# Performance work log

Measured on AMD Instinct MI355X. Metric: run time of the kernel, lower is better.

Reference implementation:

```python
import jax, jax.numpy as jnp
import numpy as np
from jax import lax

B, CIN, COUT, H, W, K = 8, 256, 256, 64, 64, 3
KK = K * K
PAD, STRIDE = 1, 1
EPS = 1e-5


def setup_inputs() -> dict:
    key = jax.random.key(0)
    k0, k1, k2 = jax.random.split(key, 3)
    x = jax.random.normal(k0, (B, CIN, H, W), jnp.float32)
    # offset/mask predicting conv: 3*K*K output channels (o1, o2, mask)
    w_off = jax.random.normal(k1, (3 * KK, CIN, K, K), jnp.float32) * 0.01
    b_off = jnp.zeros((3 * KK,), jnp.float32)
    # main deformable conv weight
    weight = jax.random.normal(k2, (COUT, CIN, K, K), jnp.float32) / np.sqrt(CIN * KK).astype(np.float32)
    bias = jnp.zeros((COUT,), jnp.float32)
    gamma = jnp.ones((COUT,), jnp.float32)
    beta = jnp.zeros((COUT,), jnp.float32)
    return {"x": x, "w_off": w_off, "b_off": b_off, "weight": weight,
            "bias": bias, "gamma": gamma, "beta": beta}


def _bilinear_sample(img, ph, pw):
    """img: [C,H,W]; ph,pw: [KK,H,W] float sample positions. Zero outside. -> [C,KK,H,W]"""
    h0 = jnp.floor(ph).astype(jnp.int32)
    w0 = jnp.floor(pw).astype(jnp.int32)
    h1, w1 = h0 + 1, w0 + 1
    lh = ph - h0.astype(ph.dtype)
    lw = pw - w0.astype(pw.dtype)
    hh, hw = 1.0 - lh, 1.0 - lw

    def corner(hi, wi):
        valid = (hi >= 0) & (hi < H) & (wi >= 0) & (wi < W)
        hc = jnp.clip(hi, 0, H - 1)
        wc = jnp.clip(wi, 0, W - 1)
        v = img[:, hc, wc]  # [C,KK,H,W]
        return v * valid.astype(img.dtype)[None]

    return (corner(h0, w0) * (hh * hw)[None] + corner(h0, w1) * (hh * lw)[None]
            + corner(h1, w0) * (lh * hw)[None] + corner(h1, w1) * (lh * lw)[None])


def _forward(x, w_off, b_off, weight, bias, gamma, beta):
    dn = ('NCHW', 'OIHW', 'NCHW')
    # offset/mask branch (standard conv)
    om = lax.conv_general_dilated(x, w_off, (STRIDE, STRIDE), ((PAD, PAD), (PAD, PAD)),
                                  dimension_numbers=dn) + b_off[None, :, None, None]
    o1, o2, m = jnp.split(om, 3, axis=1)
    offset = jnp.concatenate([o1, o2], axis=1)          # [B, 2*KK, H, W]
    off_h = offset[:, 0::2]                             # [B, KK, H, W] dy per tap
    off_w = offset[:, 1::2]                             # [B, KK, H, W] dx per tap
    mask = jax.nn.sigmoid(m)                            # [B, KK, H, W]

    taps = jnp.arange(KK)
    base_h = (taps // K - PAD).astype(jnp.float32)[:, None, None] \
        + (jnp.arange(H, dtype=jnp.float32) * STRIDE)[None, :, None]  # [KK,H,1]
    base_w = (taps % K - PAD).astype(jnp.float32)[:, None, None] \
        + (jnp.arange(W, dtype=jnp.float32) * STRIDE)[None, None, :]  # [KK,1,W]
    ph = base_h[None] + off_h                           # [B,KK,H,W]
    pw = base_w[None] + off_w

    sampled = jax.vmap(_bilinear_sample)(x, ph, pw)     # [B,CIN,KK,H,W]
    sampled = sampled * mask[:, None]                   # modulated (DCNv2)

    y = jnp.einsum('bckhw,ock->bohw', sampled, weight.reshape(COUT, CIN, KK))
    y = y + bias[None, :, None, None]

    # BatchNorm2d (training mode: batch statistics) + ReLU
    mean = y.mean(axis=(0, 2, 3))
    var = y.var(axis=(0, 2, 3))
    yn = (y - mean[None, :, None, None]) * lax.rsqrt(var + EPS)[None, :, None, None]
    out = jax.nn.relu(gamma[None, :, None, None] * yn + beta[None, :, None, None])
    return out


def reference(x, w_off, b_off, weight, bias, gamma, beta):
    return _forward(x, w_off, b_off, weight, bias, gamma, beta)
```

## Files before the change

### kernel.cpp

```cpp
#include <hip/hip_runtime.h>
#include <cstdint>

#define BB    8
#define CIN   256
#define COUT  256
#define HH    64
#define WW    64
#define HWSZ  4096
#define NPIX  32768
#define NTAP  9

typedef __attribute__((ext_vector_type(8))) short    s16x8;
typedef __attribute__((ext_vector_type(8))) unsigned short u16x8;
typedef __attribute__((ext_vector_type(4))) unsigned short u16x4;
typedef __attribute__((ext_vector_type(4))) float    f32x4;

__device__ __forceinline__ float bf2f(unsigned short u) {
    unsigned int v = ((unsigned int)u) << 16;
    return __builtin_bit_cast(float, v);
}
__device__ __forceinline__ unsigned short f2bf(float f) {
    unsigned int u = __builtin_bit_cast(unsigned int, f);
    unsigned int r = (u + 0x7FFFu + ((u >> 16) & 1u)) >> 16;
    return (unsigned short)r;
}

__global__ void k_pack_x(const float* __restrict__ x, unsigned short* __restrict__ xT) {
    int blk = blockIdx.x;
    int b    = blk & 7;
    int rest = blk >> 3;
    int h    = rest >> 2;
    int c0   = (rest & 3) * 64;
    __shared__ float tile[64][65];
    int t = threadIdx.x;
#pragma unroll
    for (int r = 0; r < 16; ++r) {
        int idx = t + r * 256;
        int i = idx >> 6, w = idx & 63;
        tile[i][w] = x[(((b * 256 + c0 + i) * 64 + h) * 64) + w];
    }
    __syncthreads();
#pragma unroll
    for (int r = 0; r < 2; ++r) {
        int idx = t + r * 256;
        int w  = idx >> 3;
        int c8 = (idx & 7) * 8;
        u16x8 res;
#pragma unroll
        for (int k = 0; k < 8; ++k) res[k] = f2bf(tile[c8 + k][w]);
        *reinterpret_cast<u16x8*>(&xT[((b * 64 + h) * 64 + w) * 256 + c0 + c8]) = res;
    }
}

__global__ void k_pack_w2(const float* __restrict__ w, const float* __restrict__ woff,
                          unsigned short* __restrict__ wT, unsigned short* __restrict__ wofT) {
    int bid = blockIdx.x;
    int t = threadIdx.x;
    if (bid < 2304) {
        int idx = bid * 256 + t;
        int j   = idx & 7;
        int q   = (idx >> 3) & 3;
        int o16 = (idx >> 5) & 15;
        int n16 = (idx >> 9) & 15;
        int kc  = (idx >> 13) & 7;
        int tp  = idx >> 16;
        int c = kc * 32 + q * 8 + j;
        int o = n16 * 16 + o16;
        wT[idx] = f2bf(w[(o * 256 + c) * 9 + tp]);
    } else {
        int idx = (bid - 2304) * 256 + t;
        int c  = idx & 255;
        int j  = (idx >> 8) & 31;
        int tp = idx >> 13;
        float v = (j < 27) ? woff[(j * 256 + c) * 9 + tp] : 0.f;
        wofT[idx] = f2bf(v);
    }
}

__global__ __launch_bounds__(256, 2)
void k_offconv(const unsigned short* __restrict__ xT,
               const unsigned short* __restrict__ wofT,
               const float* __restrict__ b_off,
               float* __restrict__ om) {
    int blk = blockIdx.x;
    int b = blk & 7, h = blk >> 3;
    int P0 = (b * 64 + h) * 64;
    int t = threadIdx.x;
    int lane = t & 63, wv = t >> 6;
    int p0w = wv * 16;
    int lm = lane & 15, q = lane >> 4;
    __shared__ unsigned short S3[3 * 66 * 136];

    const f32x4 FZ = {0.f, 0.f, 0.f, 0.f};
    f32x4 acc0 = FZ, acc1 = FZ;

    for (int cc = 0; cc < 2; ++cc) {
        __syncthreads();
        if (t < 96) {
            int rr = t >> 5, col = (t >> 4) & 1, c8 = (t & 15) * 8;
            u16x8 z = {0,0,0,0,0,0,0,0};
            *reinterpret_cast<u16x8*>(&S3[(rr * 66 + col * 65) * 136 + c8]) = z;
        }
#pragma unroll
        for (int r = 0; r < 12; ++r) {
            int v = t + r * 256;
            int rr = v >> 10, rem = v & 1023;
            int w = rem >> 4, c8 = (rem & 15) * 8;
            int hr = h + rr - 1;
            u16x8 d = {0,0,0,0,0,0,0,0};
            if (hr >= 0 && hr < 64)
                d = *reinterpret_cast<const u16x8*>(xT + ((b * 64 + hr) * 64 + w) * 256 + cc * 128 + c8);
            *reinterpret_cast<u16x8*>(&S3[(rr * 66 + w + 1) * 136 + c8]) = d;
        }
        __syncthreads();
#pragma unroll
        for (int tp = 0; tp < 9; ++tp) {
            int dh = tp / 3, dw = tp % 3;
            const unsigned short* wb = wofT + (tp * 32 + lm) * 256 + cc * 128;
#pragma unroll
            for (int kc = 0; kc < 4; ++kc) {
                s16x8 a = *reinterpret_cast<const s16x8*>(&S3[(dh * 66 + p0w + lm + dw) * 136 + kc * 32 + q * 8]);
                s16x8 b0 = *reinterpret_cast<const s16x8*>(wb + kc * 32 + q * 8);
                s16x8 b1 = *reinterpret_cast<const s16x8*>(wb + 16 * 256 + kc * 32 + q * 8);
                acc0 = __builtin_amdgcn_mfma_f32_16x16x32_bf16(a, b0, acc0, 0, 0, 0);
                acc1 = __builtin_amdgcn_mfma_f32_16x16x32_bf16(a, b1, acc1, 0, 0, 0);
            }
        }
    }
#pragma unroll
    for (int n = 0; n < 2; ++n) {
        int j = n * 16 + lm;
        float bj = (j < 27) ? b_off[j] : 0.f;
        f32x4 a = n ? acc1 : acc0;
#pragma unroll
        for (int i = 0; i < 4; ++i) {
            int prow = p0w + q * 4 + i;
            om[(P0 + prow) * 32 + j] = a[i] + bj;
        }
    }
}

__global__ __launch_bounds__(512, 4)
void k_main(const unsigned short* __restrict__ xT,
            const unsigned short* __restrict__ wTk,
            const float* __restrict__ om,
            const float* __restrict__ bias,
            unsigned short* __restrict__ y16,
            float* __restrict__ gsum, float* __restrict__ gssq) {
    int blk = blockIdx.x;
    int b = blk & 7, h = blk >> 3;
    int pblk = b * 64 + h;
    int P0 = pblk * 64;
    int t = threadIdx.x;
    int lane = t & 63, wv = t >> 6;
    int lm = lane & 15, q = lane >> 4;

    __shared__ unsigned short S[2][64 * 264];
    __shared__ float OMS[64 * 33];

    {
        int v = t * 4;
        int p = v >> 5, j = v & 31;
        float4 tmp = *reinterpret_cast<const float4*>(om + P0 * 32 + v);
        OMS[p * 33 + j]     = tmp.x;
        OMS[p * 33 + j + 1] = tmp.y;
        OMS[p * 33 + j + 2] = tmp.z;
        OMS[p * 33 + j + 3] = tmp.w;
    }
    __syncthreads();

    if (wv >= 4) {
        int pw = wv - 4;
        int s  = lane & 7;
        int pA = pw * 16 + (lane >> 3);
        int pB = pA + 8;
        int rb = b * 4096;

        float wgA[4], wgB[4];
        int   adA[4], adB[4];

        auto setup = [&](int tp, int p, float* wg, int* ad) {
            float oh = OMS[p * 33 + 2 * tp];
            float ow = OMS[p * 33 + 2 * tp + 1];
            float mv = OMS[p * 33 + 18 + tp];
            float mk = 1.f / (1.f + __expf(-mv));
            float ph = (float)(h + tp / 3 - 1) + oh;
            float pw_ = (float)(p + tp % 3 - 1) + ow;
            float fh0 = floorf(ph), fw0 = floorf(pw_);
            int ih0 = (int)fh0, iw0 = (int)fw0;
            float lh = ph - fh0, lw = pw_ - fw0;
            float hh = 1.f - lh, hw_ = 1.f - lw;
            bool vh0 = (ih0 >= 0) & (ih0 < 64);
            bool vh1 = (ih0 + 1 >= 0) & (ih0 + 1 < 64);
            bool vw0 = (iw0 >= 0) & (iw0 < 64);
            bool vw1 = (iw0 + 1 >= 0) & (iw0 + 1 < 64);
            wg[0] = hh * hw_ * mk * (float)(vh0 & vw0);
            wg[1] = hh * lw  * mk * (float)(vh0 & vw1);
            wg[2] = lh * hw_ * mk * (float)(vh1 & vw0);
            wg[3] = lh * lw  * mk * (float)(vh1 & vw1);
            int ch0 = min(max(ih0, 0), 63), ch1 = min(max(ih0 + 1, 0), 63);
            int cw0 = min(max(iw0, 0), 63), cw1 = min(max(iw0 + 1, 0), 63);
            ad[0] = ((rb + ch0 * 64 + cw0) * 256);
            ad[1] = ((rb + ch0 * 64 + cw1) * 256);
            ad[2] = ((rb + ch1 * 64 + cw0) * 256);
            ad[3] = ((rb + ch1 * 64 + cw1) * 256);
        };

        u16x8 rP[4], rQ[4];
        auto issueSet = [&](const int* ad, int j, u16x8* r) {
            int off = j * 64 + s * 8;
#pragma unroll
            for (int c = 0; c < 4; ++c)
                r[c] = *reinterpret_cast<const u16x8*>(xT + ad[c] + off);
        };
        auto blendSet = [&](int buf, int p, const float* wg, int j, u16x8* r) {
            u16x8 res;
#pragma unroll
            for (int k = 0; k < 8; ++k) {
                float v = wg[0] * bf2f(r[0][k]);
                v = fmaf(wg[1], bf2f(r[1][k]), v);
                v = fmaf(wg[2], bf2f(r[2][k]), v);
                v = fmaf(wg[3], bf2f(r[3][k]), v);
                res[k] = f2bf(v);
            }
            *reinterpret_cast<u16x8*>(&S[buf][p * 264 + j * 64 + s * 8]) = res;
        };
        auto fillTap = [&](int tp, int buf) {
            setup(tp, pA, wgA, adA);
            setup(tp, pB, wgB, adB);
            issueSet(adA, 0, rP);
            issueSet(adA, 1, rQ);
            blendSet(buf, pA, wgA, 0, rP);  issueSet(adA, 2, rP);
            blendSet(buf, pA, wgA, 1, rQ);  issueSet(adA, 3, rQ);
            blendSet(buf, pA, wgA, 2, rP);  issueSet(adB, 0, rP);
            blendSet(buf, pA, wgA, 3, rQ);  issueSet(adB, 1, rQ);
            blendSet(buf, pB, wgB, 0, rP);  issueSet(adB, 2, rP);
            blendSet(buf, pB, wgB, 1, rQ);  issueSet(adB, 3, rQ);
            blendSet(buf, pB, wgB, 2, rP);
            blendSet(buf, pB, wgB, 3, rQ);
        };

        fillTap(0, 0);
        __syncthreads();
        for (int tp = 0; tp < 9; ++tp) {
            if (tp < 8) fillTap(tp + 1, (tp + 1) & 1);
            __syncthreads();
        }
    } else {
        int o0 = wv * 64;
        const f32x4 FZ = {0.f, 0.f, 0.f, 0.f};
        f32x4 acc[4][4];
#pragma unroll
        for (int m = 0; m < 4; ++m)
#pragma unroll
            for (int n = 0; n < 4; ++n) acc[m][n] = FZ;

        __syncthreads();
        for (int tp = 0; tp < 9; ++tp) {
            const unsigned short* Sc = &S[tp & 1][0];
            const unsigned short* wtap = wTk + (size_t)tp * 65536
                                       + (size_t)(wv * 4) * 512 + lm * 32 + q * 8;
            s16x8 wbuf[2][4];
#pragma unroll
            for (int n = 0; n < 4; ++n)
                wbuf[0][n] = *reinterpret_cast<const s16x8*>(wtap + n * 512);
#pragma unroll
            for (int kc = 0; kc < 8; ++kc) {
                if (kc < 7) {
                    const unsigned short* wb = wtap + (kc + 1) * 8192;
#pragma unroll
                    for (int n = 0; n < 4; ++n)
                        wbuf[(kc + 1) & 1][n] = *reinterpret_cast<const s16x8*>(wb + n * 512);
                }
#pragma unroll
                for (int mt = 0; mt < 4; ++mt) {
                    s16x8 a = *reinterpret_cast<const s16x8*>(
                        &Sc[(mt * 16 + lm) * 264 + kc * 32 + q * 8]);
#pragma unroll
                    for (int n = 0; n < 4; ++n)
                        acc[mt][n] = __builtin_amdgcn_mfma_f32_16x16x32_bf16(
                            a, wbuf[kc & 1][n], acc[mt][n], 0, 0, 0);
                }
            }
            __syncthreads();
        }

        u16x4* yv = reinterpret_cast<u16x4*>(y16);
#pragma unroll
        for (int nt = 0; nt < 4; ++nt) {
            int o = o0 + nt * 16 + lm;
            float bo = bias[o];
            float sacc = 0.f, ssacc = 0.f;
#pragma unroll
            for (int mt = 0; mt < 4; ++mt) {
                u16x4 st;
#pragma unroll
                for (int i = 0; i < 4; ++i) {
                    float v = acc[mt][nt][i] + bo;
                    st[i] = f2bf(v);
                    sacc += v; ssacc += v * v;
                }
                int idx4 = ((pblk * 4 + wv) * 16 + nt * 4 + mt) * 64 + lane;
                yv[idx4] = st;
            }
            sacc  += __shfl_xor(sacc, 16);
            sacc  += __shfl_xor(sacc, 32);
            ssacc += __shfl_xor(ssacc, 16);
            ssacc += __shfl_xor(ssacc, 32);
            if (q == 0) {
                atomicAdd(&gsum[o], sacc);
                atomicAdd(&gssq[o], ssacc);
            }
        }
    }
}

__global__ void k_bnrelu(const unsigned short* __restrict__ y16,
                         const float* __restrict__ gsum, const float* __restrict__ gssq,
                         const float* __restrict__ gamma, const float* __restrict__ beta,
                         float* __restrict__ out) {
    int blk = blockIdx.x;
    int b = blk & 7, h = blk >> 3;
    int pblk = b * 64 + h;
    __shared__ unsigned short T[64 * 257];
    __shared__ float sc[256], sh[256];
    int t = threadIdx.x;
    {
        const float n = 32768.f;
        float mean = gsum[t] / n;
        float var = gssq[t] / n - mean * mean;
        float inv = rsqrtf(var + 1e-5f);
        float s = gamma[t] * inv;
        sc[t] = s;
        sh[t] = beta[t] - mean * s;
    }
    const u16x4* yv = reinterpret_cast<const u16x4*>(y16) + pblk * 4096;
#pragma unroll
    for (int r = 0; r < 16; ++r) {
        int v = t + r * 256;
        u16x4 d = yv[v];
        int lane = v & 63, mt = (v >> 6) & 3, nt = (v >> 8) & 3, wvv = (v >> 10) & 3;
        int p = mt * 16 + (lane >> 4) * 4;
        int o = wvv * 64 + nt * 16 + (lane & 15);
        T[(p + 0) * 257 + o] = d[0];
        T[(p + 1) * 257 + o] = d[1];
        T[(p + 2) * 257 + o] = d[2];
        T[(p + 3) * 257 + o] = d[3];
    }
    __syncthreads();
    int w4   = (t & 15) * 4;
    int orow = t >> 4;
    float* obase = out + (size_t)b * (256 * 4096) + h * 64;
#pragma unroll
    for (int it = 0; it < 16; ++it) {
        int o = orow + it * 16;
        float scl = sc[o], shf = sh[o];
        float4 vo;
        vo.x = fmaxf(bf2f(T[(w4 + 0) * 257 + o]) * scl + shf, 0.f);
        vo.y = fmaxf(bf2f(T[(w4 + 1) * 257 + o]) * scl + shf, 0.f);
        vo.z = fmaxf(bf2f(T[(w4 + 2) * 257 + o]) * scl + shf, 0.f);
        vo.w = fmaxf(bf2f(T[(w4 + 3) * 257 + o]) * scl + shf, 0.f);
        *reinterpret_cast<float4*>(obase + (size_t)o * 4096 + w4) = vo;
    }
}

extern "C" void kernel_launch(void* const* d_in, const int* in_sizes, int n_in,
                              void* d_out, int out_size, void* d_ws, size_t ws_size,
                              hipStream_t stream) {
    const float* x      = (const float*)d_in[0];
    const float* w_off  = (const float*)d_in[1];
    const float* b_off  = (const float*)d_in[2];
    const float* weight = (const float*)d_in[3];
    const float* bias   = (const float*)d_in[4];
    const float* gamma  = (const float*)d_in[5];
    const float* beta   = (const float*)d_in[6];

    char* ws = (char*)d_ws;
    const size_t OFF_XT    = 0;
    const size_t OFF_WT    = OFF_XT + 16777216;
    const size_t OFF_WOFT  = OFF_WT + 1179648;
    const size_t OFF_OM    = OFF_WOFT + 147456;
    const size_t OFF_Y16   = OFF_OM + 4194304;
    const size_t OFF_SUM   = OFF_Y16 + 16777216;
    const size_t OFF_SUMSQ = OFF_SUM + 1024;

    unsigned short* xT   = (unsigned short*)(ws + OFF_XT);
    unsigned short* wTk  = (unsigned short*)(ws + OFF_WT);
    unsigned short* wofT = (unsigned short*)(ws + OFF_WOFT);
    float* om    = (float*)(ws + OFF_OM);
    unsigned short* y16  = (unsigned short*)(ws + OFF_Y16);
    float* sum   = (float*)(ws + OFF_SUM);
    float* sumsq = (float*)(ws + OFF_SUMSQ);

    hipMemsetAsync(ws + OFF_SUM, 0, 2048, stream);

    k_pack_x <<<2048, 256, 0, stream>>>(x, xT);
    k_pack_w2<<<2592, 256, 0, stream>>>(weight, w_off, wTk, wofT);
    k_offconv<<< 512, 256, 0, stream>>>(xT, wofT, b_off, om);
    k_main   <<< 512, 512, 0, stream>>>(xT, wTk, om, bias, y16, sum, sumsq);
    k_bnrelu <<< 512, 256, 0, stream>>>(y16, sum, sumsq, gamma, beta, (float*)d_out);
}
```

Measured before the change: 211.4 us.

## Fuse offset conv into main kernel and merge pack kernels

```diff
diff --git a/kernel.cpp b/kernel.cpp
--- a/kernel.cpp
+++ b/kernel.cpp
@@ -6,9 +6,6 @@
 #define COUT  256
 #define HH    64
 #define WW    64
-#define HWSZ  4096
-#define NPIX  32768
-#define NTAP  9
 
 typedef __attribute__((ext_vector_type(8))) short    s16x8;
 typedef __attribute__((ext_vector_type(8))) unsigned short u16x8;
@@ -25,39 +22,39 @@
     return (unsigned short)r;
 }
 
-__global__ void k_pack_x(const float* __restrict__ x, unsigned short* __restrict__ xT) {
+__global__ void k_pack(const float* __restrict__ x,
+                       const float* __restrict__ w,
+                       const float* __restrict__ woff,
+                       unsigned short* __restrict__ xT,
+                       unsigned short* __restrict__ wTk,
+                       unsigned short* __restrict__ wofT) {
     int blk = blockIdx.x;
-    int b    = blk & 7;
-    int rest = blk >> 3;
-    int h    = rest >> 2;
-    int c0   = (rest & 3) * 64;
-    __shared__ float tile[64][65];
     int t = threadIdx.x;
-#pragma unroll
-    for (int r = 0; r < 16; ++r) {
-        int idx = t + r * 256;
-        int i = idx >> 6, w = idx & 63;
-        tile[i][w] = x[(((b * 256 + c0 + i) * 64 + h) * 64) + w];
-    }
-    __syncthreads();
-#pragma unroll
-    for (int r = 0; r < 2; ++r) {
-        int idx = t + r * 256;
-        int w  = idx >> 3;
-        int c8 = (idx & 7) * 8;
-        u16x8 res;
-#pragma unroll
-        for (int k = 0; k < 8; ++k) res[k] = f2bf(tile[c8 + k][w]);
-        *reinterpret_cast<u16x8*>(&xT[((b * 64 + h) * 64 + w) * 256 + c0 + c8]) = res;
-    }
-}
-
-__global__ void k_pack_w2(const float* __restrict__ w, const float* __restrict__ woff,
-                          unsigned short* __restrict__ wT, unsigned short* __restrict__ wofT) {
-    int bid = blockIdx.x;
-    int t = threadIdx.x;
-    if (bid < 2304) {
-        int idx = bid * 256 + t;
+    __shared__ float tile[64 * 65];
+    if (blk < 2048) {
+        int b    = blk & 7;
+        int rest = blk >> 3;
+        int h    = rest >> 2;
+        int c0   = (rest & 3) * 64;
+#pragma unroll
+        for (int r = 0; r < 16; ++r) {
+            int idx = t + r * 256;
+            int i = idx >> 6, w_ = idx & 63;
+            tile[i * 65 + w_] = x[(((b * 256 + c0 + i) * 64 + h) * 64) + w_];
+        }
+        __syncthreads();
+#pragma unroll
+        for (int r = 0; r < 2; ++r) {
+            int idx = t + r * 256;
+            int w_ = idx >> 3;
+            int c8 = (idx & 7) * 8;
+            u16x8 res;
+#pragma unroll
+            for (int k = 0; k < 8; ++k) res[k] = f2bf(tile[(c8 + k) * 65 + w_]);
+            *reinterpret_cast<u16x8*>(&xT[((b * 64 + h) * 64 + w_) * 256 + c0 + c8]) = res;
+        }
+    } else if (blk < 4352) {
+        int idx = (blk - 2048) * 256 + t;
         int j   = idx & 7;
         int q   = (idx >> 3) & 3;
         int o16 = (idx >> 5) & 15;
@@ -66,108 +63,95 @@
         int tp  = idx >> 16;
         int c = kc * 32 + q * 8 + j;
         int o = n16 * 16 + o16;
-        wT[idx] = f2bf(w[(o * 256 + c) * 9 + tp]);
+        wTk[idx] = f2bf(w[(o * 256 + c) * 9 + tp]);
     } else {
-        int idx = (bid - 2304) * 256 + t;
+        int idx = (blk - 4352) * 256 + t;
         int c  = idx & 255;
         int j  = (idx >> 8) & 31;
         int tp = idx >> 13;
-        float v = (j < 27) ? woff[(j * 256 + c) * 9 + tp] : 0.f;
-        wofT[idx] = f2bf(v);
-    }
-}
-
-__global__ __launch_bounds__(256, 2)
-void k_offconv(const unsigned short* __restrict__ xT,
-               const unsigned short* __restrict__ wofT,
-               const float* __restrict__ b_off,
-               float* __restrict__ om) {
-    int blk = blockIdx.x;
-    int b = blk & 7, h = blk >> 3;
-    int P0 = (b * 64 + h) * 64;
-    int t = threadIdx.x;
-    int lane = t & 63, wv = t >> 6;
-    int p0w = wv * 16;
-    int lm = lane & 15, q = lane >> 4;
-    __shared__ unsigned short S3[3 * 66 * 136];
-
-    const f32x4 FZ = {0.f, 0.f, 0.f, 0.f};
-    f32x4 acc0 = FZ, acc1 = FZ;
-
-    for (int cc = 0; cc < 2; ++cc) {
-        __syncthreads();
-        if (t < 96) {
-            int rr = t >> 5, col = (t >> 4) & 1, c8 = (t & 15) * 8;
-            u16x8 z = {0,0,0,0,0,0,0,0};
-            *reinterpret_cast<u16x8*>(&S3[(rr * 66 + col * 65) * 136 + c8]) = z;
-        }
-#pragma unroll
-        for (int r = 0; r < 12; ++r) {
-            int v = t + r * 256;
-            int rr = v >> 10, rem = v & 1023;
-            int w = rem >> 4, c8 = (rem & 15) * 8;
-            int hr = h + rr - 1;
-            u16x8 d = {0,0,0,0,0,0,0,0};
-            if (hr >= 0 && hr < 64)
-                d = *reinterpret_cast<const u16x8*>(xT + ((b * 64 + hr) * 64 + w) * 256 + cc * 128 + c8);
-            *reinterpret_cast<u16x8*>(&S3[(rr * 66 + w + 1) * 136 + c8]) = d;
-        }
-        __syncthreads();
-#pragma unroll
-        for (int tp = 0; tp < 9; ++tp) {
-            int dh = tp / 3, dw = tp % 3;
-            const unsigned short* wb = wofT + (tp * 32 + lm) * 256 + cc * 128;
-#pragma unroll
-            for (int kc = 0; kc < 4; ++kc) {
-                s16x8 a = *reinterpret_cast<const s16x8*>(&S3[(dh * 66 + p0w + lm + dw) * 136 + kc * 32 + q * 8]);
-                s16x8 b0 = *reinterpret_cast<const s16x8*>(wb + kc * 32 + q * 8);
-                s16x8 b1 = *reinterpret_cast<const s16x8*>(wb + 16 * 256 + kc * 32 + q * 8);
-                acc0 = __builtin_amdgcn_mfma_f32_16x16x32_bf16(a, b0, acc0, 0, 0, 0);
-                acc1 = __builtin_amdgcn_mfma_f32_16x16x32_bf16(a, b1, acc1, 0, 0, 0);
-            }
-        }
-    }
-#pragma unroll
-    for (int n = 0; n < 2; ++n) {
-        int j = n * 16 + lm;
-        float bj = (j < 27) ? b_off[j] : 0.f;
-        f32x4 a = n ? acc1 : acc0;
-#pragma unroll
-        for (int i = 0; i < 4; ++i) {
-            int prow = p0w + q * 4 + i;
-            om[(P0 + prow) * 32 + j] = a[i] + bj;
-        }
+        wofT[idx] = f2bf((j < 27) ? woff[(j * 256 + c) * 9 + tp] : 0.f);
     }
 }
 
 __global__ __launch_bounds__(512, 4)
 void k_main(const unsigned short* __restrict__ xT,
             const unsigned short* __restrict__ wTk,
-            const float* __restrict__ om,
+            const unsigned short* __restrict__ wofT,
+            const float* __restrict__ boffg,
             const float* __restrict__ bias,
             unsigned short* __restrict__ y16,
             float* __restrict__ gsum, float* __restrict__ gssq) {
+    __shared__ __align__(16) char smem[76032];
     int blk = blockIdx.x;
     int b = blk & 7, h = blk >> 3;
     int pblk = b * 64 + h;
-    int P0 = pblk * 64;
     int t = threadIdx.x;
     int lane = t & 63, wv = t >> 6;
     int lm = lane & 15, q = lane >> 4;
-
-    __shared__ unsigned short S[2][64 * 264];
-    __shared__ float OMS[64 * 33];
+    const f32x4 FZ = {0.f, 0.f, 0.f, 0.f};
 
     {
-        int v = t * 4;
-        int p = v >> 5, j = v & 31;
-        float4 tmp = *reinterpret_cast<const float4*>(om + P0 * 32 + v);
-        OMS[p * 33 + j]     = tmp.x;
-        OMS[p * 33 + j + 1] = tmp.y;
-        OMS[p * 33 + j + 2] = tmp.z;
-        OMS[p * 33 + j + 3] = tmp.w;
-    }
-    __syncthreads();
+        unsigned short* S3 = (unsigned short*)smem;
+        float* OMS = (float*)(smem + 67584);
+        f32x4 oacc0 = FZ, oacc1 = FZ;
+        int p0w = wv * 16;
+        for (int cc = 0; cc < 2; ++cc) {
+            __syncthreads();
+            if (t < 96) {
+                int rr = t >> 5, col = (t >> 4) & 1, c8 = (t & 15) * 8;
+                u16x8 z = {0,0,0,0,0,0,0,0};
+                *reinterpret_cast<u16x8*>(&S3[(rr * 66 + col * 65) * 136 + c8]) = z;
+            }
+#pragma unroll
+            for (int r = 0; r < 6; ++r) {
+                int v = t + r * 512;
+                int rr = v >> 10, rem = v & 1023;
+                int w_ = rem >> 4, c8 = (rem & 15) * 8;
+                int hr = h + rr - 1;
+                u16x8 d = {0,0,0,0,0,0,0,0};
+                if (hr >= 0 && hr < 64)
+                    d = *reinterpret_cast<const u16x8*>(xT + ((b * 64 + hr) * 64 + w_) * 256 + cc * 128 + c8);
+                *reinterpret_cast<u16x8*>(&S3[(rr * 66 + w_ + 1) * 136 + c8]) = d;
+            }
+            __syncthreads();
+            if (wv < 4) {
+#pragma unroll
+                for (int tp = 0; tp < 9; ++tp) {
+                    int dh = tp / 3, dw = tp % 3;
+                    const unsigned short* wb = wofT + (tp * 32 + lm) * 256 + cc * 128;
+#pragma unroll
+                    for (int kc = 0; kc < 4; ++kc) {
+                        s16x8 a = *reinterpret_cast<const s16x8*>(
+                            &S3[(dh * 66 + p0w + lm + dw) * 136 + kc * 32 + q * 8]);
+                        s16x8 b0 = *reinterpret_cast<const s16x8*>(wb + kc * 32 + q * 8);
+                        s16x8 b1 = *reinterpret_cast<const s16x8*>(wb + 16 * 256 + kc * 32 + q * 8);
+                        oacc0 = __builtin_amdgcn_mfma_f32_16x16x32_bf16(a, b0, oacc0, 0, 0, 0);
+                        oacc1 = __builtin_amdgcn_mfma_f32_16x16x32_bf16(a, b1, oacc1, 0, 0, 0);
+                    }
+                }
+            }
+        }
+        if (wv < 4) {
+#pragma unroll
+            for (int n = 0; n < 2; ++n) {
+                int j = n * 16 + lm;
+                float bj = (j < 27) ? boffg[j] : 0.f;
+                f32x4 a = n ? oacc1 : oacc0;
+#pragma unroll
+                for (int i = 0; i < 4; ++i)
+                    OMS[(p0w + q * 4 + i) * 33 + j] = a[i] + bj;
+            }
+        }
+        __syncthreads();
+    }
+
+    unsigned short* S = (unsigned short*)smem;
+    float* OMS = (float*)(smem + 67584);
+    f32x4 acc[4][4];
+#pragma unroll
+    for (int m = 0; m < 4; ++m)
+#pragma unroll
+        for (int n = 0; n < 4; ++n) acc[m][n] = FZ;
 
     if (wv >= 4) {
         int pw = wv - 4;
@@ -179,7 +163,7 @@
         float wgA[4], wgB[4];
         int   adA[4], adB[4];
 
-        auto setup = [&](int tp, int p, float* wg, int* ad) {
+        auto setup = [&](int tp, int p, float* wgt, int* ad) {
             float oh = OMS[p * 33 + 2 * tp];
             float ow = OMS[p * 33 + 2 * tp + 1];
             float mv = OMS[p * 33 + 18 + tp];
@@ -194,10 +178,10 @@
             bool vh1 = (ih0 + 1 >= 0) & (ih0 + 1 < 64);
             bool vw0 = (iw0 >= 0) & (iw0 < 64);
             bool vw1 = (iw0 + 1 >= 0) & (iw0 + 1 < 64);
-            wg[0] = hh * hw_ * mk * (float)(vh0 & vw0);
-            wg[1] = hh * lw  * mk * (float)(vh0 & vw1);
-            wg[2] = lh * hw_ * mk * (float)(vh1 & vw0);
-            wg[3] = lh * lw  * mk * (float)(vh1 & vw1);
+            wgt[0] = hh * hw_ * mk * (float)(vh0 & vw0);
+            wgt[1] = hh * lw  * mk * (float)(vh0 & vw1);
+            wgt[2] = lh * hw_ * mk * (float)(vh1 & vw0);
+            wgt[3] = lh * lw  * mk * (float)(vh1 & vw1);
             int ch0 = min(max(ih0, 0), 63), ch1 = min(max(ih0 + 1, 0), 63);
             int cw0 = min(max(iw0, 0), 63), cw1 = min(max(iw0 + 1, 0), 63);
             ad[0] = ((rb + ch0 * 64 + cw0) * 256);
@@ -213,17 +197,17 @@
             for (int c = 0; c < 4; ++c)
                 r[c] = *reinterpret_cast<const u16x8*>(xT + ad[c] + off);
         };
-        auto blendSet = [&](int buf, int p, const float* wg, int j, u16x8* r) {
+        auto blendSet = [&](int buf, int p, const float* wgt, int j, u16x8* r) {
             u16x8 res;
 #pragma unroll
             for (int k = 0; k < 8; ++k) {
-                float v = wg[0] * bf2f(r[0][k]);
-                v = fmaf(wg[1], bf2f(r[1][k]), v);
-                v = fmaf(wg[2], bf2f(r[2][k]), v);
-                v = fmaf(wg[3], bf2f(r[3][k]), v);
+                float v = wgt[0] * bf2f(r[0][k]);
+                v = fmaf(wgt[1], bf2f(r[1][k]), v);
+                v = fmaf(wgt[2], bf2f(r[2][k]), v);
+                v = fmaf(wgt[3], bf2f(r[3][k]), v);
                 res[k] = f2bf(v);
             }
-            *reinterpret_cast<u16x8*>(&S[buf][p * 264 + j * 64 + s * 8]) = res;
+            *reinterpret_cast<u16x8*>(&S[buf * 16896 + p * 264 + j * 64 + s * 8]) = res;
         };
         auto fillTap = [&](int tp, int buf) {
             setup(tp, pA, wgA, adA);
@@ -247,17 +231,9 @@
             __syncthreads();
         }
     } else {
-        int o0 = wv * 64;
-        const f32x4 FZ = {0.f, 0.f, 0.f, 0.f};
-        f32x4 acc[4][4];
-#pragma unroll
-        for (int m = 0; m < 4; ++m)
-#pragma unroll
-            for (int n = 0; n < 4; ++n) acc[m][n] = FZ;
-
         __syncthreads();
         for (int tp = 0; tp < 9; ++tp) {
-            const unsigned short* Sc = &S[tp & 1][0];
+            const unsigned short* Sc = &S[(tp & 1) * 16896];
             const unsigned short* wtap = wTk + (size_t)tp * 65536
                                        + (size_t)(wv * 4) * 512 + lm * 32 + q * 8;
             s16x8 wbuf[2][4];
@@ -284,11 +260,13 @@
             }
             __syncthreads();
         }
-
+    }
+
+    if (wv < 4) {
         u16x4* yv = reinterpret_cast<u16x4*>(y16);
 #pragma unroll
         for (int nt = 0; nt < 4; ++nt) {
-            int o = o0 + nt * 16 + lm;
+            int o = wv * 64 + nt * 16 + lm;
             float bo = bias[o];
             float sacc = 0.f, ssacc = 0.f;
 #pragma unroll
@@ -379,24 +357,20 @@
     const size_t OFF_XT    = 0;
     const size_t OFF_WT    = OFF_XT + 16777216;
     const size_t OFF_WOFT  = OFF_WT + 1179648;
-    const size_t OFF_OM    = OFF_WOFT + 147456;
-    const size_t OFF_Y16   = OFF_OM + 4194304;
+    const size_t OFF_Y16   = OFF_WOFT + 147456;
     const size_t OFF_SUM   = OFF_Y16 + 16777216;
     const size_t OFF_SUMSQ = OFF_SUM + 1024;
 
     unsigned short* xT   = (unsigned short*)(ws + OFF_XT);
     unsigned short* wTk  = (unsigned short*)(ws + OFF_WT);
     unsigned short* wofT = (unsigned short*)(ws + OFF_WOFT);
-    float* om    = (float*)(ws + OFF_OM);
     unsigned short* y16  = (unsigned short*)(ws + OFF_Y16);
-    float* sum   = (float*)(ws + OFF_SUM);
-    float* sumsq = (float*)(ws + OFF_SUMSQ);
+    float* gsum  = (float*)(ws + OFF_SUM);
+    float* gssq  = (float*)(ws + OFF_SUMSQ);
 
     hipMemsetAsync(ws + OFF_SUM, 0, 2048, stream);
 
-    k_pack_x <<<2048, 256, 0, stream>>>(x, xT);
-    k_pack_w2<<<2592, 256, 0, stream>>>(weight, w_off, wTk, wofT);
-    k_offconv<<< 512, 256, 0, stream>>>(xT, wofT, b_off, om);
-    k_main   <<< 512, 512, 0, stream>>>(xT, wTk, om, bias, y16, sum, sumsq);
-    k_bnrelu <<< 512, 256, 0, stream>>>(y16, sum, sumsq, gamma, beta, (float*)d_out);
-}
+    k_pack  <<<4640, 256, 0, stream>>>(x, weight, w_off, xT, wTk, wofT);
+    k_main  <<< 512, 512, 0, stream>>>(xT, wTk, wofT, b_off, bias, y16, gsum, gssq);
+    k_bnrelu<<< 512, 256, 0, stream>>>(y16, gsum, gssq, gamma, beta, (float*)d_out);
+}
```

After: 207.2 us. -2.0%, faster.
